# Optimization experiments

Hardware: AMD Instinct MI355X
Metric: run time of the kernel (lower is better)

## Reference

```python
import jax, jax.numpy as jnp
import numpy as np

B, S, F_DIM, H = 2, 2048, 1024, 16
DH = F_DIM // H  # 64


def setup_inputs() -> dict:
    key = jax.random.key(0)
    ks = jax.random.split(key, 12)
    scale = 1.0 / np.sqrt(F_DIM)
    inp = {
        "Q": jax.random.normal(ks[0], (B, S, F_DIM), jnp.float32),
        "K": jax.random.normal(ks[1], (B, S, F_DIM), jnp.float32),
        "V": jax.random.normal(ks[2], (B, S, F_DIM), jnp.float32),
        "mask": jnp.zeros((1, 1, S, S), jnp.float32),
        "Wq": jax.random.uniform(ks[3], (F_DIM, F_DIM), jnp.float32, -scale, scale),
        "bq": jax.random.uniform(ks[4], (F_DIM,), jnp.float32, -scale, scale),
        "Wk": jax.random.uniform(ks[5], (F_DIM, F_DIM), jnp.float32, -scale, scale),
        "bk": jax.random.uniform(ks[6], (F_DIM,), jnp.float32, -scale, scale),
        "Wv": jax.random.uniform(ks[7], (F_DIM, F_DIM), jnp.float32, -scale, scale),
        "bv": jax.random.uniform(ks[8], (F_DIM,), jnp.float32, -scale, scale),
        "Wo": jax.random.uniform(ks[9], (F_DIM, F_DIM), jnp.float32, -scale, scale),
        "bo": jax.random.uniform(ks[10], (F_DIM,), jnp.float32, -scale, scale),
    }
    return inp


def _split_heads(x):
    # [B, S, F] -> [B, H, S, DH]
    b, s, _ = x.shape
    return x.reshape(b, s, H, DH).transpose(0, 2, 1, 3)


def reference(Q, K, V, mask, Wq, bq, Wk, bk, Wv, bv, Wo, bo):
    q = _split_heads(Q @ Wq.T + bq)  # [B, H, S, DH]
    k = _split_heads(K @ Wk.T + bk)
    v = _split_heads(V @ Vv_fix(Wv).T + bv) if False else _split_heads(V @ Wv.T + bv)
    scores = jnp.einsum("bhqd,bhkd->bhqk", q, k) / jnp.sqrt(jnp.float32(DH))
    scores = scores + mask
    probs = jax.nn.softmax(scores, axis=-1)
    attn = jnp.einsum("bhqk,bhkd->bhqd", probs, v)  # [B, H, S, DH]
    out = attn.transpose(0, 2, 1, 3).reshape(Q.shape[0], Q.shape[1], F_DIM)
    return out @ Wo.T + bo
```

## Files before the change

### kernel.cpp

```cpp
#include <hip/hip_runtime.h>
#include <hip/hip_bf16.h>

typedef unsigned short u16;
typedef unsigned int u32;
typedef __attribute__((ext_vector_type(4))) float f32x4;
typedef __attribute__((ext_vector_type(16))) float f32x16;
typedef __attribute__((ext_vector_type(8))) short short8;
typedef __attribute__((ext_vector_type(4))) u32 u32x4;

#define SEQ 2048
#define FD  1024
#define NH  16
#define DHD 64

__device__ __forceinline__ u16 f2bf(float f) {
  __hip_bfloat16 h = __float2bfloat16(f);
  return *reinterpret_cast<u16*>(&h);
}
__device__ __forceinline__ u32 pack2bf(float lo, float hi) {
  return (u32)f2bf(lo) | ((u32)f2bf(hi) << 16);
}

#define GLOAD_LDS16(gp, lp)                                        \
  __builtin_amdgcn_global_load_lds(                                \
      (const __attribute__((address_space(1))) unsigned int*)(gp), \
      (__attribute__((address_space(3))) unsigned int*)(lp), 16, 0, 0)

__global__ __launch_bounds__(256) void prep_kernel(
    const float* __restrict__ Q, const float* __restrict__ K, const float* __restrict__ V,
    const float* __restrict__ Wq, const float* __restrict__ Wk, const float* __restrict__ Wv,
    const float* __restrict__ Wo, const float* __restrict__ mask,
    u16* __restrict__ Abf, u16* __restrict__ Wbf, u32* __restrict__ flag) {
  const size_t i = ((size_t)blockIdx.x * 256 + threadIdx.x) * 8;
  if (i >= 16777216) {
    const u32* mp = (const u32*)mask + (i - 16777216);
    u32x4 a = *reinterpret_cast<const u32x4*>(mp);
    u32x4 b = *reinterpret_cast<const u32x4*>(mp + 4);
    u32 o = a[0] | a[1] | a[2] | a[3] | b[0] | b[1] | b[2] | b[3];
    if (__ballot(o != 0) != 0ull && (threadIdx.x & 63) == 0) atomicOr(flag, 1u);
    return;
  }
  const float* src;
  u16* dst;
  if (i < 12582912) {
    const int s = (int)(i >> 22);
    const size_t off = i & 0x3FFFFF;
    src = (s == 0 ? Q : s == 1 ? K : V) + off;
    dst = Abf + i;
  } else {
    const size_t j = i - 12582912;
    const int w = (int)(j >> 20);
    const size_t off = j & 0xFFFFF;
    src = (w == 0 ? Wq : w == 1 ? Wk : w == 2 ? Wv : Wo) + off;
    dst = Wbf + j;
  }
  f32x4 a = *reinterpret_cast<const f32x4*>(src);
  f32x4 b = *reinterpret_cast<const f32x4*>(src + 4);
  union { u32 u[4]; short8 s; } pk;
  pk.u[0] = pack2bf(a[0], a[1]); pk.u[1] = pack2bf(a[2], a[3]);
  pk.u[2] = pack2bf(b[0], b[1]); pk.u[3] = pack2bf(b[2], b[3]);
  *reinterpret_cast<short8*>(dst) = pk.s;
}

__device__ __forceinline__ void gemm128_bf16(const u16* __restrict__ A, const u16* __restrict__ W,
                                             int m0, int n0, u16* As, u16* Bs,
                                             f32x4 (&acc)[4][4]) {
  const int tid = threadIdx.x, lane = tid & 63, wv = tid >> 6;
  const int wr = (tid >> 7) & 1, wc = (tid >> 6) & 1;
  const int lr = lane & 15, lk = (lane >> 4) << 3;
  const int srow = lane >> 2;
  const int scol = (lane & 3) << 3;
#pragma unroll
  for (int m = 0; m < 4; ++m)
#pragma unroll
    for (int n = 0; n < 4; ++n) acc[m][n] = {0.f, 0.f, 0.f, 0.f};

  for (int k0 = 0; k0 < FD; k0 += 32) {
    __syncthreads();
#pragma unroll
    for (int c = 0; c < 2; ++c) {
      GLOAD_LDS16(&A[(size_t)(m0 + c * 64 + wv * 16 + srow) * FD + k0 + scol],
                  &As[(c * 64 + wv * 16) * 32]);
      GLOAD_LDS16(&W[(size_t)(n0 + c * 64 + wv * 16 + srow) * FD + k0 + scol],
                  &Bs[(c * 64 + wv * 16) * 32]);
    }
    __syncthreads();
    short8 a[4], b[4];
#pragma unroll
    for (int m = 0; m < 4; ++m)
      a[m] = *reinterpret_cast<const short8*>(&As[(wr * 64 + m * 16 + lr) * 32 + lk]);
#pragma unroll
    for (int n = 0; n < 4; ++n)
      b[n] = *reinterpret_cast<const short8*>(&Bs[(wc * 64 + n * 16 + lr) * 32 + lk]);
#pragma unroll
    for (int m = 0; m < 4; ++m)
#pragma unroll
      for (int n = 0; n < 4; ++n)
        acc[m][n] = __builtin_amdgcn_mfma_f32_16x16x32_bf16(a[m], b[n], acc[m][n], 0, 0, 0);
  }
}

__global__ __launch_bounds__(256) void proj_qkv_kernel(
    const u16* __restrict__ Abf, const u16* __restrict__ Wbf,
    const float* __restrict__ bq, const float* __restrict__ bk, const float* __restrict__ bv,
    u16* __restrict__ qh, u16* __restrict__ kh, u16* __restrict__ vF) {
  __shared__ u16 As[128 * 32];
  __shared__ u16 Bs[128 * 32];
  const int bid = blockIdx.x;
  const int which = bid >> 8;
  const int rr = bid & 255;
  const int slot = rr >> 3;
  const int y = (rr & 7) + 8 * (slot & 3);
  const int x = slot >> 2;
  const int m0 = y * 128, n0 = x * 128;
  const u16* A = Abf + ((size_t)which << 22);
  const u16* W = Wbf + ((size_t)which << 20);
  const float* bias = (which == 0) ? bq : (which == 1) ? bk : bv;
  const float qscale = 0.18033688011112042f;

  f32x4 acc[4][4];
  gemm128_bf16(A, W, m0, n0, As, Bs, acc);

  u16* out = (which == 0) ? qh : (which == 1) ? kh : vF;
  const int lane = threadIdx.x & 63;
  const int wr = (threadIdx.x >> 7) & 1, wc = (threadIdx.x >> 6) & 1;
  const int rbase = m0 + wr * 64 + ((lane >> 4) << 2);
  const int cbase = n0 + wc * 64 + (lane & 15);
#pragma unroll
  for (int n = 0; n < 4; ++n) {
    const int col = cbase + n * 16;
    const float bvv = bias[col];
    const int h = col >> 6, dh = col & 63;
#pragma unroll
    for (int m = 0; m < 4; ++m) {
#pragma unroll
      for (int r = 0; r < 4; ++r) {
        const int row = rbase + m * 16 + r;
        const int b = row >> 11, s = row & 2047;
        float v = acc[m][n][r] + bvv;
        if (which == 0) v *= qscale;
        const size_t bhbase = (size_t)(b * 16 + h) * SEQ * DHD;
        size_t idx;
        if (which == 0) {
          idx = bhbase + (size_t)s * 64 + dh;
        } else if (which == 1) {
          idx = bhbase + ((size_t)(((s >> 5) * 4 + (dh >> 4)) * 64
                          + ((dh >> 3) & 1) * 32 + (s & 31)) << 3) + (dh & 7);
        } else {
          idx = bhbase + ((size_t)(((s >> 4) * 2 + (dh >> 5)) * 64
                          + ((s >> 3) & 1) * 32 + (dh & 31)) << 3) + (s & 7);
        }
        out[idx] = f2bf(v);
      }
    }
  }
}

__device__ __forceinline__ void load_ktile(const u16* __restrict__ kp, int kv0, int lane,
                                           short8 (&kf)[8]) {
#pragma unroll
  for (int h2 = 0; h2 < 2; ++h2)
#pragma unroll
    for (int d = 0; d < 4; ++d)
      kf[h2 * 4 + d] = *reinterpret_cast<const short8*>(
          &kp[((size_t)((((kv0 >> 5) + h2) * 4 + d) * 64 + lane)) << 3]);
}

__device__ __forceinline__ void attn_tile(
    const short8 (&kf)[8], const u16* __restrict__ vp, const float* __restrict__ mrow,
    u32 has_mask, int kv0, int lane, int hi, const short8 (&qf)[4],
    f32x16 (&oacc)[2], float& m2, float& lsum) {
  const float L2E = 1.44269504088896340736f;
  short8 vf[8];
#pragma unroll
  for (int kb = 0; kb < 4; ++kb)
#pragma unroll
    for (int db = 0; db < 2; ++db)
      vf[kb * 2 + db] = *reinterpret_cast<const short8*>(
          &vp[((size_t)((((kv0 >> 4) + kb) * 2 + db) * 64 + lane)) << 3]);

  f32x16 st[2];
#pragma unroll
  for (int h2 = 0; h2 < 2; ++h2) {
    f32x16 z;
#pragma unroll
    for (int e = 0; e < 16; ++e) z[e] = 0.f;
#pragma unroll
    for (int d = 0; d < 4; ++d)
      z = __builtin_amdgcn_mfma_f32_32x32x16_bf16(kf[h2 * 4 + d], qf[d], z, 0, 0, 0);
    st[h2] = z;
  }
  float p[32];
  if (__builtin_expect(has_mask != 0, 0)) {
#pragma unroll
    for (int h2 = 0; h2 < 2; ++h2)
#pragma unroll
      for (int g = 0; g < 4; ++g) {
        f32x4 mv = *reinterpret_cast<const f32x4*>(&mrow[kv0 + h2 * 32 + g * 8 + hi * 4]);
#pragma unroll
        for (int j = 0; j < 4; ++j)
          p[h2 * 16 + g * 4 + j] = fmaf(mv[j], L2E, st[h2][g * 4 + j]);
      }
  } else {
#pragma unroll
    for (int h2 = 0; h2 < 2; ++h2)
#pragma unroll
      for (int e = 0; e < 16; ++e) p[h2 * 16 + e] = st[h2][e];
  }
  float t8[8];
#pragma unroll
  for (int i = 0; i < 8; ++i)
    t8[i] = fmaxf(fmaxf(p[i], p[i + 8]), fmaxf(p[i + 16], p[i + 24]));
#pragma unroll
  for (int i = 0; i < 4; ++i) t8[i] = fmaxf(t8[i], t8[i + 4]);
  float mt = fmaxf(fmaxf(t8[0], t8[1]), fmaxf(t8[2], t8[3]));
  mt = fmaxf(mt, __shfl_xor(mt, 32));
  const float mnew = fmaxf(m2, mt);
  const float alpha = __builtin_amdgcn_exp2f(m2 - mnew);
  m2 = mnew;
#pragma unroll
  for (int i = 0; i < 32; ++i) p[i] = __builtin_amdgcn_exp2f(p[i] - m2);
  float s8[8];
#pragma unroll
  for (int i = 0; i < 8; ++i) s8[i] = (p[i] + p[i + 8]) + (p[i + 16] + p[i + 24]);
#pragma unroll
  for (int i = 0; i < 4; ++i) s8[i] += s8[i + 4];
  float ssum = (s8[0] + s8[1]) + (s8[2] + s8[3]);
  ssum += __shfl_xor(ssum, 32);
  lsum = lsum * alpha + ssum;
#pragma unroll
  for (int e = 0; e < 16; ++e) { oacc[0][e] *= alpha; oacc[1][e] *= alpha; }

#pragma unroll
  for (int kb = 0; kb < 4; ++kb) {
    const int pb = (kb >> 1) * 16 + (kb & 1) * 8;
    u32 x = pack2bf(p[pb + 0], p[pb + 1]);
    u32 y = pack2bf(p[pb + 4], p[pb + 5]);
    asm volatile("v_permlane32_swap_b32 %0, %1" : "+v"(x), "+v"(y));
    u32 zz = pack2bf(p[pb + 2], p[pb + 3]);
    u32 w = pack2bf(p[pb + 6], p[pb + 7]);
    asm volatile("v_permlane32_swap_b32 %0, %1" : "+v"(zz), "+v"(w));
    union { u32 u[4]; short8 s; } bf;
    bf.u[0] = x; bf.u[1] = zz; bf.u[2] = y; bf.u[3] = w;
#pragma unroll
    for (int db = 0; db < 2; ++db)
      oacc[db] = __builtin_amdgcn_mfma_f32_32x32x16_bf16(vf[kb * 2 + db], bf.s, oacc[db], 0, 0, 0);
  }
}

__global__ __launch_bounds__(256, 2) void attn_kernel(
    const u16* __restrict__ qh, const u16* __restrict__ kh, const u16* __restrict__ vF,
    const float* __restrict__ mask, const u32* __restrict__ mflag, u16* __restrict__ O) {
  const int wave = threadIdx.x >> 6, lane = threadIdx.x & 63;
  const int bid = blockIdx.x;
  const int vid = (bid & 7) * 64 + (bid >> 3);
  const int bh = vid >> 4;
  const int q0 = (vid & 15) * 128 + wave * 32;
  const int lq = lane & 31;
  const int hi = lane >> 5;
  const u16* qp = qh + (size_t)bh * SEQ * DHD;
  const u16* kp = kh + (size_t)bh * SEQ * DHD;
  const u16* vp = vF + (size_t)bh * SEQ * DHD;
  const float* mrow = mask + (size_t)(q0 + lq) * SEQ;
  const u32 has_mask = *mflag;

  short8 qf[4];
#pragma unroll
  for (int d = 0; d < 4; ++d)
    qf[d] = *reinterpret_cast<const short8*>(&qp[(size_t)(q0 + lq) * DHD + d * 16 + hi * 8]);

  f32x16 oacc[2];
#pragma unroll
  for (int e = 0; e < 16; ++e) { oacc[0][e] = 0.f; oacc[1][e] = 0.f; }
  float m2 = -INFINITY, lsum = 0.f;

  short8 ka[8], kb2[8];
  load_ktile(kp, 0, lane, ka);
  for (int it = 0; it < 32; it += 2) {
    const int kv0 = it << 6;
    load_ktile(kp, kv0 + 64, lane, kb2);
    attn_tile(ka, vp, mrow, has_mask, kv0, lane, hi, qf, oacc, m2, lsum);
    load_ktile(kp, (it == 30) ? 0 : kv0 + 128, lane, ka);
    attn_tile(kb2, vp, mrow, has_mask, kv0 + 64, lane, hi, qf, oacc, m2, lsum);
  }

  const int b = bh >> 4, h = bh & 15;
  const float inv = 1.0f / lsum;
  u16* orow = O + ((size_t)(b * SEQ + q0 + lq) * NH + h) * DHD;
#pragma unroll
  for (int db = 0; db < 2; ++db)
#pragma unroll
    for (int g = 0; g < 4; ++g) {
      union { u16 u[4]; unsigned long long ll; } pk;
#pragma unroll
      for (int j = 0; j < 4; ++j) pk.u[j] = f2bf(oacc[db][g * 4 + j] * inv);
      *reinterpret_cast<unsigned long long*>(&orow[db * 32 + g * 8 + hi * 4]) = pk.ll;
    }
}

__global__ __launch_bounds__(256) void out_proj_kernel(
    const u16* __restrict__ O, const u16* __restrict__ WoB, const float* __restrict__ bo,
    float* __restrict__ out) {
  __shared__ u16 As[128 * 32];
  __shared__ u16 Bs[128 * 32];
  const int rr = blockIdx.x;
  const int slot = rr >> 3;
  const int y = (rr & 7) + 8 * (slot & 3);
  const int x = slot >> 2;
  const int m0 = y * 128, n0 = x * 128;
  f32x4 acc[4][4];
  gemm128_bf16(O, WoB, m0, n0, As, Bs, acc);

  const int lane = threadIdx.x & 63;
  const int wr = (threadIdx.x >> 7) & 1, wc = (threadIdx.x >> 6) & 1;
  const int rbase = m0 + wr * 64 + ((lane >> 4) << 2);
  const int cbase = n0 + wc * 64 + (lane & 15);
#pragma unroll
  for (int n = 0; n < 4; ++n) {
    const int col = cbase + n * 16;
    const float bvv = bo[col];
#pragma unroll
    for (int m = 0; m < 4; ++m)
#pragma unroll
      for (int r = 0; r < 4; ++r) {
        const int row = rbase + m * 16 + r;
        out[(size_t)row * FD + col] = acc[m][n][r] + bvv;
      }
  }
}

extern "C" void kernel_launch(void* const* d_in, const int* in_sizes, int n_in,
                              void* d_out, int out_size, void* d_ws, size_t ws_size,
                              hipStream_t stream) {
  (void)in_sizes; (void)n_in; (void)out_size; (void)ws_size;
  const float* Q    = (const float*)d_in[0];
  const float* K    = (const float*)d_in[1];
  const float* V    = (const float*)d_in[2];
  const float* mask = (const float*)d_in[3];
  const float* Wq   = (const float*)d_in[4];
  const float* bq   = (const float*)d_in[5];
  const float* Wk   = (const float*)d_in[6];
  const float* bk   = (const float*)d_in[7];
  const float* Wv   = (const float*)d_in[8];
  const float* bv   = (const float*)d_in[9];
  const float* Wo   = (const float*)d_in[10];
  const float* bo   = (const float*)d_in[11];
  float* out = (float*)d_out;

  u16* ws = (u16*)d_ws;
  const size_t SZ = (size_t)4096 * 1024;
  u16* qh  = ws;
  u16* kh  = qh + SZ;
  u16* vF  = kh + SZ;
  u16* O   = vF + SZ;
  u16* Abf = O + SZ;
  u16* Wbf = Abf + 3 * SZ;
  u32* mflag = (u32*)(Wbf + 4 * (size_t)1024 * 1024);

  hipMemsetAsync(mflag, 0, 4, stream);
  prep_kernel<<<dim3(10240), 256, 0, stream>>>(Q, K, V, Wq, Wk, Wv, Wo, mask, Abf, Wbf, mflag);

  proj_qkv_kernel<<<dim3(768), 256, 0, stream>>>(Abf, Wbf, bq, bk, bv, qh, kh, vF);

  attn_kernel<<<dim3(512), 256, 0, stream>>>(qh, kh, vF, mask, mflag, O);

  out_proj_kernel<<<dim3(256), 256, 0, stream>>>(O, Wbf + 3 * (size_t)1024 * 1024, bo, out);
}
```

Measured before the change: 142.3 us.

## Split attention KV range across wave pairs and merge partials in LDS

Each block now covers 64 query rows with two waves per 32-row group, each wave handling half of the key/value sequence; partial max, sum and output are merged through shared memory at the end. The grid doubles to 1024 blocks and launch bounds rise to 4 blocks per CU, aiming for more parallelism and latency hiding. It also skips the online-softmax rescale when the running max grows by no more than a threshold, uses the hardware packed bf16 convert, and raises wave priority around MFMA sections. The costs are an extra LDS reduction with two barriers, possible register pressure under the tighter launch bound, and a small numerical risk from the lazy rescale.

```diff
diff --git a/kernel.cpp b/kernel.cpp
--- a/kernel.cpp
+++ b/kernel.cpp
@@ -19,6 +19,11 @@
 }
 __device__ __forceinline__ u32 pack2bf(float lo, float hi) {
   return (u32)f2bf(lo) | ((u32)f2bf(hi) << 16);
+}
+__device__ __forceinline__ u32 cvtpk(float lo, float hi) {
+  u32 r;
+  asm("v_cvt_pk_bf16_f32 %0, %1, %2" : "=v"(r) : "v"(lo), "v"(hi));
+  return r;
 }
 
 #define GLOAD_LDS16(gp, lp)                                        \
@@ -180,6 +185,7 @@
           &vp[((size_t)((((kv0 >> 4) + kb) * 2 + db) * 64 + lane)) << 3]);
 
   f32x16 st[2];
+  __builtin_amdgcn_s_setprio(1);
 #pragma unroll
   for (int h2 = 0; h2 < 2; ++h2) {
     f32x16 z;
@@ -190,6 +196,7 @@
       z = __builtin_amdgcn_mfma_f32_32x32x16_bf16(kf[h2 * 4 + d], qf[d], z, 0, 0, 0);
     st[h2] = z;
   }
+  __builtin_amdgcn_s_setprio(0);
   float p[32];
   if (__builtin_expect(has_mask != 0, 0)) {
 #pragma unroll
@@ -215,9 +222,14 @@
   for (int i = 0; i < 4; ++i) t8[i] = fmaxf(t8[i], t8[i + 4]);
   float mt = fmaxf(fmaxf(t8[0], t8[1]), fmaxf(t8[2], t8[3]));
   mt = fmaxf(mt, __shfl_xor(mt, 32));
-  const float mnew = fmaxf(m2, mt);
-  const float alpha = __builtin_amdgcn_exp2f(m2 - mnew);
-  m2 = mnew;
+  if (!__all(mt - m2 <= 8.f)) {
+    const float mnew = fmaxf(m2, mt);
+    const float alpha = __builtin_amdgcn_exp2f(m2 - mnew);
+    m2 = mnew;
+    lsum *= alpha;
+#pragma unroll
+    for (int e = 0; e < 16; ++e) { oacc[0][e] *= alpha; oacc[1][e] *= alpha; }
+  }
 #pragma unroll
   for (int i = 0; i < 32; ++i) p[i] = __builtin_amdgcn_exp2f(p[i] - m2);
   float s8[8];
@@ -227,18 +239,17 @@
   for (int i = 0; i < 4; ++i) s8[i] += s8[i + 4];
   float ssum = (s8[0] + s8[1]) + (s8[2] + s8[3]);
   ssum += __shfl_xor(ssum, 32);
-  lsum = lsum * alpha + ssum;
-#pragma unroll
-  for (int e = 0; e < 16; ++e) { oacc[0][e] *= alpha; oacc[1][e] *= alpha; }
-
+  lsum += ssum;
+
+  __builtin_amdgcn_s_setprio(1);
 #pragma unroll
   for (int kb = 0; kb < 4; ++kb) {
     const int pb = (kb >> 1) * 16 + (kb & 1) * 8;
-    u32 x = pack2bf(p[pb + 0], p[pb + 1]);
-    u32 y = pack2bf(p[pb + 4], p[pb + 5]);
+    u32 x = cvtpk(p[pb + 0], p[pb + 1]);
+    u32 y = cvtpk(p[pb + 4], p[pb + 5]);
     asm volatile("v_permlane32_swap_b32 %0, %1" : "+v"(x), "+v"(y));
-    u32 zz = pack2bf(p[pb + 2], p[pb + 3]);
-    u32 w = pack2bf(p[pb + 6], p[pb + 7]);
+    u32 zz = cvtpk(p[pb + 2], p[pb + 3]);
+    u32 w = cvtpk(p[pb + 6], p[pb + 7]);
     asm volatile("v_permlane32_swap_b32 %0, %1" : "+v"(zz), "+v"(w));
     union { u32 u[4]; short8 s; } bf;
     bf.u[0] = x; bf.u[1] = zz; bf.u[2] = y; bf.u[3] = w;
@@ -246,16 +257,20 @@
     for (int db = 0; db < 2; ++db)
       oacc[db] = __builtin_amdgcn_mfma_f32_32x32x16_bf16(vf[kb * 2 + db], bf.s, oacc[db], 0, 0, 0);
   }
-}
-
-__global__ __launch_bounds__(256, 2) void attn_kernel(
+  __builtin_amdgcn_s_setprio(0);
+}
+
+__global__ __launch_bounds__(256, 4) void attn_kernel(
     const u16* __restrict__ qh, const u16* __restrict__ kh, const u16* __restrict__ vF,
     const float* __restrict__ mask, const u32* __restrict__ mflag, u16* __restrict__ O) {
+  __shared__ float red[2][2][2][32];
+  __shared__ float osum[2][32][68];
   const int wave = threadIdx.x >> 6, lane = threadIdx.x & 63;
+  const int qgrp = wave >> 1, half = wave & 1;
   const int bid = blockIdx.x;
-  const int vid = (bid & 7) * 64 + (bid >> 3);
-  const int bh = vid >> 4;
-  const int q0 = (vid & 15) * 128 + wave * 32;
+  const int vid = (bid & 7) * 128 + (bid >> 3);
+  const int bh = vid >> 5;
+  const int q0 = (vid & 31) * 64 + qgrp * 32;
   const int lq = lane & 31;
   const int hi = lane >> 5;
   const u16* qp = qh + (size_t)bh * SEQ * DHD;
@@ -274,28 +289,51 @@
   for (int e = 0; e < 16; ++e) { oacc[0][e] = 0.f; oacc[1][e] = 0.f; }
   float m2 = -INFINITY, lsum = 0.f;
 
+  const int kvb = half * (SEQ / 2);
   short8 ka[8], kb2[8];
-  load_ktile(kp, 0, lane, ka);
-  for (int it = 0; it < 32; it += 2) {
-    const int kv0 = it << 6;
+  load_ktile(kp, kvb, lane, ka);
+  for (int it = 0; it < 16; it += 2) {
+    const int kv0 = kvb + (it << 6);
     load_ktile(kp, kv0 + 64, lane, kb2);
     attn_tile(ka, vp, mrow, has_mask, kv0, lane, hi, qf, oacc, m2, lsum);
-    load_ktile(kp, (it == 30) ? 0 : kv0 + 128, lane, ka);
+    load_ktile(kp, (it == 14) ? kvb : kv0 + 128, lane, ka);
     attn_tile(kb2, vp, mrow, has_mask, kv0 + 64, lane, hi, qf, oacc, m2, lsum);
   }
 
-  const int b = bh >> 4, h = bh & 15;
-  const float inv = 1.0f / lsum;
-  u16* orow = O + ((size_t)(b * SEQ + q0 + lq) * NH + h) * DHD;
-#pragma unroll
-  for (int db = 0; db < 2; ++db)
-#pragma unroll
-    for (int g = 0; g < 4; ++g) {
-      union { u16 u[4]; unsigned long long ll; } pk;
-#pragma unroll
-      for (int j = 0; j < 4; ++j) pk.u[j] = f2bf(oacc[db][g * 4 + j] * inv);
-      *reinterpret_cast<unsigned long long*>(&orow[db * 32 + g * 8 + hi * 4]) = pk.ll;
-    }
+  if (hi == 0) { red[qgrp][half][0][lq] = m2; red[qgrp][half][1][lq] = lsum; }
+  __syncthreads();
+  const float Mfin = fmaxf(red[qgrp][0][0][lq], red[qgrp][1][0][lq]);
+  const float beta = __builtin_amdgcn_exp2f(m2 - Mfin);
+  const float mo = red[qgrp][half ^ 1][0][lq];
+  const float lo = red[qgrp][half ^ 1][1][lq];
+  const float ltot = lsum * beta + lo * __builtin_amdgcn_exp2f(mo - Mfin);
+#pragma unroll
+  for (int e = 0; e < 16; ++e) { oacc[0][e] *= beta; oacc[1][e] *= beta; }
+  if (half == 0) {
+#pragma unroll
+    for (int db = 0; db < 2; ++db)
+#pragma unroll
+      for (int g = 0; g < 4; ++g) {
+        f32x4 v = {oacc[db][g * 4], oacc[db][g * 4 + 1], oacc[db][g * 4 + 2], oacc[db][g * 4 + 3]};
+        *reinterpret_cast<f32x4*>(&osum[qgrp][lq][db * 32 + g * 8 + hi * 4]) = v;
+      }
+  }
+  __syncthreads();
+  if (half == 1) {
+    const int b = bh >> 4, h = bh & 15;
+    const float inv = 1.0f / ltot;
+    u16* orow = O + ((size_t)(b * SEQ + q0 + lq) * NH + h) * DHD;
+#pragma unroll
+    for (int db = 0; db < 2; ++db)
+#pragma unroll
+      for (int g = 0; g < 4; ++g) {
+        f32x4 s = *reinterpret_cast<const f32x4*>(&osum[qgrp][lq][db * 32 + g * 8 + hi * 4]);
+        union { u32 u[2]; unsigned long long ll; } pk;
+        pk.u[0] = cvtpk((s[0] + oacc[db][g * 4 + 0]) * inv, (s[1] + oacc[db][g * 4 + 1]) * inv);
+        pk.u[1] = cvtpk((s[2] + oacc[db][g * 4 + 2]) * inv, (s[3] + oacc[db][g * 4 + 3]) * inv);
+        *reinterpret_cast<unsigned long long*>(&orow[db * 32 + g * 8 + hi * 4]) = pk.ll;
+      }
+  }
 }
 
 __global__ __launch_bounds__(256) void out_proj_kernel(
@@ -362,7 +400,7 @@
 
   proj_qkv_kernel<<<dim3(768), 256, 0, stream>>>(Abf, Wbf, bq, bk, bv, qh, kh, vF);
 
-  attn_kernel<<<dim3(512), 256, 0, stream>>>(qh, kh, vF, mask, mflag, O);
+  attn_kernel<<<dim3(1024), 256, 0, stream>>>(qh, kh, vF, mask, mflag, O);
 
   out_proj_kernel<<<dim3(256), 256, 0, stream>>>(O, Wbf + 3 * (size_t)1024 * 1024, bo, out);
 }
```

New measurement: 392.8 us. +176.0%, slower.
